# Kernel tuning notes

Hardware: AMD Instinct MI355X
Metric: run time of the kernel (lower is better)

Reference implementation:

```python
import jax, jax.numpy as jnp
import numpy as np

IN_CH = 4
HIDDEN = 64
N_NODES = 2048   # nodes per graph
B = 8            # graphs in batch
TOTAL_N = B * N_NODES
N_EDGES = 524288
MAX_NEIGH = 15


def glorot(key, shape):
    lim = float(np.sqrt(6.0 / (shape[0] + shape[1])))
    return jax.random.uniform(key, shape, jnp.float32, -lim, lim)


def setup_inputs() -> dict:
    key = jax.random.key(0)
    ks = jax.random.split(key, 10)
    x = jax.random.normal(ks[0], (TOTAL_N, IN_CH), jnp.float32)
    edge_index = jax.random.randint(ks[1], (2, N_EDGES), 0, TOTAL_N, jnp.int64)
    return {
        "x": x,
        "edge_index": edge_index,
        "W1": glorot(ks[2], (IN_CH, HIDDEN)),
        "b1": jnp.zeros((HIDDEN,), jnp.float32),
        "W2": glorot(ks[3], (HIDDEN, HIDDEN)),
        "b2": jnp.zeros((HIDDEN,), jnp.float32),
        "Wf1": glorot(ks[4], (N_NODES * HIDDEN, N_NODES)),
        "bf1": jnp.zeros((N_NODES,), jnp.float32),
        "Wf2": glorot(ks[5], (N_NODES, MAX_NEIGH)),
        "bf2": jnp.zeros((MAX_NEIGH,), jnp.float32),
    }


def gcn_conv(x, W, b, src, dst, num_nodes):
    """PyG GCNConv: add self-loops, symmetric D^-1/2 (A+I) D^-1/2 normalization."""
    h = x @ W  # [N, out]
    loop = jnp.arange(num_nodes, dtype=src.dtype)
    s = jnp.concatenate([src, loop])
    d = jnp.concatenate([dst, loop])
    deg = jax.ops.segment_sum(jnp.ones(s.shape, h.dtype), d, num_segments=num_nodes)
    dis = jnp.where(deg > 0, jax.lax.rsqrt(jnp.maximum(deg, 1e-12)), 0.0)
    norm = dis[s] * dis[d]  # [E+N]
    out = jax.ops.segment_sum(h[s] * norm[:, None], d, num_segments=num_nodes)
    return out + b


def reference(x, edge_index, W1, b1, W2, b2, Wf1, bf1, Wf2, bf2):
    src, dst = edge_index[0], edge_index[1]
    h = jax.nn.selu(gcn_conv(x, W1, b1, src, dst, TOTAL_N))
    h = jax.nn.selu(gcn_conv(h, W2, b2, src, dst, TOTAL_N))
    h = h.reshape(-1, N_NODES * HIDDEN)          # [B, n_nodes*hidden]
    h = jax.nn.selu(h @ Wf1 + bf1)               # [B, n_nodes]
    return h @ Wf2 + bf2                         # [B, max_n_neighbors]
```

## Files before the change

kernel.cpp:

```cpp
#include <hip/hip_runtime.h>
#include <cstdint>
#include <cstddef>

#define E_EDGES     524288
#define N_TOT       16384
#define HID         64
#define B_GR        8
#define KTOT        131072
#define NJ          2048
#define MAXN        15
#define SLOTS       96

#define KC          256
#define NCHUNK      512

typedef float vf4 __attribute__((ext_vector_type(4)));

#define OFF_CURSOR  0x0u
#define OFF_DIS     0x10000u
#define OFF_SLOTS   0x20000u
#define OFF_H1      0x320000u
#define OFF_H2      0x720000u
#define OFF_TMP     0xB20000u
#define OFF_PART    0xBA0000u

__device__ __forceinline__ float selu_f(float x) {
    const float scale = 1.0507009873554805f;
    const float alpha = 1.6732632423543772f;
    return x > 0.0f ? scale * x : scale * alpha * expm1f(x);
}

__global__ void scatter_kernel(const int* __restrict__ src, const int* __restrict__ dst,
                               int* __restrict__ cursor, unsigned short* __restrict__ slots) {
    int e = blockIdx.x * 256 + threadIdx.x;
    if (e >= E_EDGES) return;
    int s = src[e], d = dst[e];
    int pos = atomicAdd(&cursor[d], 1);
    slots[d * SLOTS + pos] = (unsigned short)s;
}

__global__ void dis_kernel(const int* __restrict__ cursor, float* __restrict__ dis) {
    int i = blockIdx.x * 256 + threadIdx.x;
    if (i < N_TOT) dis[i] = rsqrtf((float)(cursor[i] + 1));
}

__launch_bounds__(256)
__global__ void gather1_kernel(const int* __restrict__ cursor,
                               const unsigned short* __restrict__ slots,
                               const float* __restrict__ dis, const float* __restrict__ x,
                               const float* __restrict__ W1, const float* __restrict__ b1,
                               float* __restrict__ h1) {
    int node = blockIdx.x * 4 + (threadIdx.x >> 6);
    int c = threadIdx.x & 63;
    float w0 = W1[c], w1 = W1[64 + c], w2 = W1[128 + c], w3 = W1[192 + c];
    int deg = cursor[node];
    float ds = dis[node];
    const unsigned short* sl = slots + node * SLOTS;
    float acc = 0.f;
    int i = 0;
    for (; i + 1 < deg; i += 2) {
        int sa = sl[i], sb = sl[i + 1];
        float da = dis[sa], db = dis[sb];
        const float4 xa = *reinterpret_cast<const float4*>(x + (size_t)sa * 4);
        const float4 xb = *reinterpret_cast<const float4*>(x + (size_t)sb * 4);
        float xwa = fmaf(xa.x, w0, fmaf(xa.y, w1, fmaf(xa.z, w2, xa.w * w3)));
        float xwb = fmaf(xb.x, w0, fmaf(xb.y, w1, fmaf(xb.z, w2, xb.w * w3)));
        acc = fmaf(xwa, da, acc);
        acc = fmaf(xwb, db, acc);
    }
    if (i < deg) {
        int sa = sl[i];
        float da = dis[sa];
        const float4 xa = *reinterpret_cast<const float4*>(x + (size_t)sa * 4);
        float xwa = fmaf(xa.x, w0, fmaf(xa.y, w1, fmaf(xa.z, w2, xa.w * w3)));
        acc = fmaf(xwa, da, acc);
    }
    const float4 xd = *reinterpret_cast<const float4*>(x + (size_t)node * 4);
    float xwd = fmaf(xd.x, w0, fmaf(xd.y, w1, fmaf(xd.z, w2, xd.w * w3)));
    float val = fmaf(acc, ds, xwd * ds * ds) + b1[c];
    h1[(size_t)node * HID + c] = selu_f(val);
}

__launch_bounds__(256)
__global__ void agg2h2_kernel(const int* __restrict__ cursor,
                              const unsigned short* __restrict__ slots,
                              const float* __restrict__ dis, const float* __restrict__ h1,
                              const float* __restrict__ W2, const float* __restrict__ b2,
                              float* __restrict__ h2) {
    __shared__ float w2s[HID * HID];
    for (int idx = threadIdx.x; idx < HID * HID; idx += 256) w2s[idx] = W2[idx];
    __syncthreads();

    int node = blockIdx.x * 4 + (threadIdx.x >> 6);
    int c = threadIdx.x & 63;
    int deg = cursor[node];
    float ds = dis[node];
    const unsigned short* sl = slots + node * SLOTS;
    float acc = 0.f;
    int i = 0;
    for (; i + 3 < deg; i += 4) {
        int sa = sl[i], sb = sl[i + 1], sc = sl[i + 2], sd = sl[i + 3];
        float da = dis[sa], db = dis[sb], dc = dis[sc], dd = dis[sd];
        acc = fmaf(h1[(size_t)sa * HID + c], da, acc);
        acc = fmaf(h1[(size_t)sb * HID + c], db, acc);
        acc = fmaf(h1[(size_t)sc * HID + c], dc, acc);
        acc = fmaf(h1[(size_t)sd * HID + c], dd, acc);
    }
    for (; i < deg; ++i) {
        int sa = sl[i];
        acc = fmaf(h1[(size_t)sa * HID + c], dis[sa], acc);
    }
    size_t base = (size_t)node * HID + c;
    float inv = acc * ds + h1[base] * ds * ds;

    float o = b2[c];
    #pragma unroll
    for (int cc = 0; cc < HID; ++cc)
        o = fmaf(__shfl(inv, cc, 64), w2s[cc * HID + c], o);
    h2[base] = selu_f(o);
}

__launch_bounds__(512, 4)
__global__ void fc1_kernel(const float* __restrict__ h2, const float* __restrict__ Wf1,
                           float* __restrict__ partials) {
    __shared__ float hch[B_GR * KC];
    const int chunk = blockIdx.x;
    const int k0 = chunk * KC;
    for (int idx = threadIdx.x; idx < B_GR * KC; idx += 512) {
        int b = idx >> 8;
        int kk = idx & (KC - 1);
        hch[idx] = h2[(size_t)b * KTOT + k0 + kk];
    }
    __syncthreads();
    vf4 acc[B_GR];
    #pragma unroll
    for (int b = 0; b < B_GR; ++b) acc[b] = (vf4)(0.f);
    const int j = threadIdx.x * 4;
    const float* wp = Wf1 + (size_t)k0 * NJ + j;
    #pragma unroll 4
    for (int kk4 = 0; kk4 < KC / 4; ++kk4) {
        vf4 w0 = __builtin_nontemporal_load(reinterpret_cast<const vf4*>(wp));
        vf4 w1 = __builtin_nontemporal_load(reinterpret_cast<const vf4*>(wp + NJ));
        vf4 w2 = __builtin_nontemporal_load(reinterpret_cast<const vf4*>(wp + 2 * NJ));
        vf4 w3 = __builtin_nontemporal_load(reinterpret_cast<const vf4*>(wp + 3 * NJ));
        wp += 4 * NJ;
        #pragma unroll
        for (int b = 0; b < B_GR; ++b) {
            const vf4 hv = *reinterpret_cast<const vf4*>(&hch[b * KC + kk4 * 4]);
            acc[b] += w0 * hv.x;
            acc[b] += w1 * hv.y;
            acc[b] += w2 * hv.z;
            acc[b] += w3 * hv.w;
        }
    }
    float* pp = partials + (size_t)chunk * (B_GR * NJ) + j;
    #pragma unroll
    for (int b = 0; b < B_GR; ++b)
        *reinterpret_cast<vf4*>(pp + (size_t)b * NJ) = acc[b];
}

__global__ void fc1_reduce1_kernel(const float* __restrict__ partials, float* __restrict__ tmp) {
    int idx = blockIdx.x * 256 + threadIdx.x;
    int g = blockIdx.y;
    float s = 0.f;
    const float* p = partials + (size_t)(g * 64) * (B_GR * NJ) + idx;
    #pragma unroll 8
    for (int c = 0; c < 64; ++c) { s += *p; p += B_GR * NJ; }
    tmp[(size_t)g * (B_GR * NJ) + idx] = s;
}

__global__ void fc2_kernel(const float* __restrict__ tmp, const float* __restrict__ bf1,
                           const float* __restrict__ Wf2, const float* __restrict__ bf2,
                           float* __restrict__ out) {
    int b = blockIdx.x;
    int t = threadIdx.x;
    float acc[MAXN];
    #pragma unroll
    for (int m = 0; m < MAXN; ++m) acc[m] = 0.f;
    for (int j = t; j < NJ; j += 64) {
        size_t o = (size_t)b * NJ + j;
        float s = 0.f;
        #pragma unroll
        for (int g = 0; g < 8; ++g) s += tmp[(size_t)g * (B_GR * NJ) + o];
        float zv = selu_f(s + bf1[j]);
        const float* wr = Wf2 + (size_t)j * MAXN;
        #pragma unroll
        for (int m = 0; m < MAXN; ++m) acc[m] = fmaf(zv, wr[m], acc[m]);
    }
    #pragma unroll
    for (int m = 0; m < MAXN; ++m) {
        float v = acc[m];
        for (int off = 32; off > 0; off >>= 1) v += __shfl_down(v, off, 64);
        if (t == 0) out[b * MAXN + m] = v + bf2[m];
    }
}

extern "C" void kernel_launch(void* const* d_in, const int* in_sizes, int n_in,
                              void* d_out, int out_size, void* d_ws, size_t ws_size,
                              hipStream_t stream) {
    const float* x    = (const float*)d_in[0];
    const int*   ei   = (const int*)d_in[1];
    const float* W1   = (const float*)d_in[2];
    const float* b1   = (const float*)d_in[3];
    const float* W2   = (const float*)d_in[4];
    const float* b2   = (const float*)d_in[5];
    const float* Wf1  = (const float*)d_in[6];
    const float* bf1  = (const float*)d_in[7];
    const float* Wf2  = (const float*)d_in[8];
    const float* bf2  = (const float*)d_in[9];
    float* out = (float*)d_out;

    const int* src = ei;
    const int* dst = ei + E_EDGES;

    char* ws = (char*)d_ws;
    int*            cursor = (int*)            (ws + OFF_CURSOR);
    float*          dis    = (float*)          (ws + OFF_DIS);
    unsigned short* slots  = (unsigned short*) (ws + OFF_SLOTS);
    float*          h1     = (float*)          (ws + OFF_H1);
    float*          h2     = (float*)          (ws + OFF_H2);
    float*          tmp    = (float*)          (ws + OFF_TMP);
    float*          parts  = (float*)          (ws + OFF_PART);

    (void)hipMemsetAsync(cursor, 0, N_TOT * sizeof(int), stream);

    scatter_kernel<<<E_EDGES / 256, 256, 0, stream>>>(src, dst, cursor, slots);
    dis_kernel<<<N_TOT / 256, 256, 0, stream>>>(cursor, dis);
    gather1_kernel<<<N_TOT / 4, 256, 0, stream>>>(cursor, slots, dis, x, W1, b1, h1);
    agg2h2_kernel<<<N_TOT / 4, 256, 0, stream>>>(cursor, slots, dis, h1, W2, b2, h2);
    fc1_kernel <<<NCHUNK, 512, 0, stream>>>(h2, Wf1, parts);
    fc1_reduce1_kernel<<<dim3(64, 8), 256, 0, stream>>>(parts, tmp);
    fc2_kernel <<<B_GR, 64, 0, stream>>>(tmp, bf1, Wf2, bf2, out);
}
```

Before: 295.9 us.

## Fuse second GCN aggregation and W2 transform into FC1 chunk kernel

The second GCN layer (neighbor aggregation plus the 64x64 W2 transform and SELU) is now computed inside the FC1 kernel. Each block produces exactly the 4 nodes per graph that its K-chunk needs and writes them straight into shared memory. This removes one kernel launch and the h2 write/read round trip through global memory. The cost is that the irregular gather work now runs at 512 blocks of 512 threads with 4 reps per warp, which may give less latency hiding than the old 4096-block launch and delays the Wf1 streaming in each block.

Result: slower. 361.8 us (+22.3%).

```diff
diff --git a/kernel.cpp b/kernel.cpp
--- a/kernel.cpp
+++ b/kernel.cpp
@@ -20,9 +20,8 @@
 #define OFF_DIS     0x10000u
 #define OFF_SLOTS   0x20000u
 #define OFF_H1      0x320000u
-#define OFF_H2      0x720000u
-#define OFF_TMP     0xB20000u
-#define OFF_PART    0xBA0000u
+#define OFF_TMP     0x720000u
+#define OFF_PART    0x7A0000u
 
 __device__ __forceinline__ float selu_f(float x) {
     const float scale = 1.0507009873554805f;
@@ -81,61 +80,60 @@
     h1[(size_t)node * HID + c] = selu_f(val);
 }
 
-__launch_bounds__(256)
-__global__ void agg2h2_kernel(const int* __restrict__ cursor,
-                              const unsigned short* __restrict__ slots,
-                              const float* __restrict__ dis, const float* __restrict__ h1,
-                              const float* __restrict__ W2, const float* __restrict__ b2,
-                              float* __restrict__ h2) {
+__launch_bounds__(512, 4)
+__global__ void fc1_fused_kernel(const int* __restrict__ cursor,
+                                 const unsigned short* __restrict__ slots,
+                                 const float* __restrict__ dis, const float* __restrict__ h1,
+                                 const float* __restrict__ W2, const float* __restrict__ b2,
+                                 const float* __restrict__ Wf1,
+                                 float* __restrict__ partials) {
     __shared__ float w2s[HID * HID];
-    for (int idx = threadIdx.x; idx < HID * HID; idx += 256) w2s[idx] = W2[idx];
-    __syncthreads();
-
-    int node = blockIdx.x * 4 + (threadIdx.x >> 6);
-    int c = threadIdx.x & 63;
-    int deg = cursor[node];
-    float ds = dis[node];
-    const unsigned short* sl = slots + node * SLOTS;
-    float acc = 0.f;
-    int i = 0;
-    for (; i + 3 < deg; i += 4) {
-        int sa = sl[i], sb = sl[i + 1], sc = sl[i + 2], sd = sl[i + 3];
-        float da = dis[sa], db = dis[sb], dc = dis[sc], dd = dis[sd];
-        acc = fmaf(h1[(size_t)sa * HID + c], da, acc);
-        acc = fmaf(h1[(size_t)sb * HID + c], db, acc);
-        acc = fmaf(h1[(size_t)sc * HID + c], dc, acc);
-        acc = fmaf(h1[(size_t)sd * HID + c], dd, acc);
-    }
-    for (; i < deg; ++i) {
-        int sa = sl[i];
-        acc = fmaf(h1[(size_t)sa * HID + c], dis[sa], acc);
-    }
-    size_t base = (size_t)node * HID + c;
-    float inv = acc * ds + h1[base] * ds * ds;
-
-    float o = b2[c];
-    #pragma unroll
-    for (int cc = 0; cc < HID; ++cc)
-        o = fmaf(__shfl(inv, cc, 64), w2s[cc * HID + c], o);
-    h2[base] = selu_f(o);
-}
-
-__launch_bounds__(512, 4)
-__global__ void fc1_kernel(const float* __restrict__ h2, const float* __restrict__ Wf1,
-                           float* __restrict__ partials) {
     __shared__ float hch[B_GR * KC];
     const int chunk = blockIdx.x;
+    const int tid = threadIdx.x;
+
+    for (int idx = tid; idx < HID * HID; idx += 512) w2s[idx] = W2[idx];
+    __syncthreads();
+
+    {
+        int w = tid >> 6, c = tid & 63;
+        #pragma unroll
+        for (int rep = 0; rep < 4; ++rep) {
+            int p = w + rep * 8;
+            int b = p >> 2, l = p & 3;
+            int g = b * 2048 + chunk * 4 + l;
+            int deg = cursor[g];
+            float ds = dis[g];
+            const unsigned short* sl = slots + g * SLOTS;
+            float acc = 0.f;
+            int i = 0;
+            for (; i + 3 < deg; i += 4) {
+                int sa = sl[i], sb = sl[i + 1], sc = sl[i + 2], sd = sl[i + 3];
+                float da = dis[sa], db = dis[sb], dc = dis[sc], dd = dis[sd];
+                acc = fmaf(h1[(size_t)sa * HID + c], da, acc);
+                acc = fmaf(h1[(size_t)sb * HID + c], db, acc);
+                acc = fmaf(h1[(size_t)sc * HID + c], dc, acc);
+                acc = fmaf(h1[(size_t)sd * HID + c], dd, acc);
+            }
+            for (; i < deg; ++i) {
+                int sa = sl[i];
+                acc = fmaf(h1[(size_t)sa * HID + c], dis[sa], acc);
+            }
+            float inv = acc * ds + h1[(size_t)g * HID + c] * ds * ds;
+            float o = b2[c];
+            #pragma unroll
+            for (int cc = 0; cc < HID; ++cc)
+                o = fmaf(__shfl(inv, cc, 64), w2s[cc * HID + c], o);
+            hch[b * KC + l * 64 + c] = selu_f(o);
+        }
+    }
+    __syncthreads();
+
     const int k0 = chunk * KC;
-    for (int idx = threadIdx.x; idx < B_GR * KC; idx += 512) {
-        int b = idx >> 8;
-        int kk = idx & (KC - 1);
-        hch[idx] = h2[(size_t)b * KTOT + k0 + kk];
-    }
-    __syncthreads();
     vf4 acc[B_GR];
     #pragma unroll
     for (int b = 0; b < B_GR; ++b) acc[b] = (vf4)(0.f);
-    const int j = threadIdx.x * 4;
+    const int j = tid * 4;
     const float* wp = Wf1 + (size_t)k0 * NJ + j;
     #pragma unroll 4
     for (int kk4 = 0; kk4 < KC / 4; ++kk4) {
@@ -218,7 +216,6 @@
     float*          dis    = (float*)          (ws + OFF_DIS);
     unsigned short* slots  = (unsigned short*) (ws + OFF_SLOTS);
     float*          h1     = (float*)          (ws + OFF_H1);
-    float*          h2     = (float*)          (ws + OFF_H2);
     float*          tmp    = (float*)          (ws + OFF_TMP);
     float*          parts  = (float*)          (ws + OFF_PART);
 
@@ -227,8 +224,7 @@
     scatter_kernel<<<E_EDGES / 256, 256, 0, stream>>>(src, dst, cursor, slots);
     dis_kernel<<<N_TOT / 256, 256, 0, stream>>>(cursor, dis);
     gather1_kernel<<<N_TOT / 4, 256, 0, stream>>>(cursor, slots, dis, x, W1, b1, h1);
-    agg2h2_kernel<<<N_TOT / 4, 256, 0, stream>>>(cursor, slots, dis, h1, W2, b2, h2);
-    fc1_kernel <<<NCHUNK, 512, 0, stream>>>(h2, Wf1, parts);
+    fc1_fused_kernel<<<NCHUNK, 512, 0, stream>>>(cursor, slots, dis, h1, W2, b2, Wf1, parts);
     fc1_reduce1_kernel<<<dim3(64, 8), 256, 0, stream>>>(parts, tmp);
     fc2_kernel <<<B_GR, 64, 0, stream>>>(tmp, bf1, Wf2, bf2, out);
 }
```
